# Kernel optimization log

Measured on AMD Instinct MI355X. Metric: run time of the kernel, lower is better.

Reference implementation:

```python
import jax, jax.numpy as jnp
import numpy as np
import math

# Static config derived from init_kwargs
B, L, D, H, NL = 256, 256, 128, 2, 2
E = D // H                       # 64
F = L // 2 + 1                   # 129 rfft bins
SR = 0.6                         # sample_ratio (> 1/n_layers)
STEP = (F * (1.0 - SR)) // (NL - 1)          # 51.0, python float floor-div as in torch code
LEFTS = [int(F * (1.0 - SR) - k * STEP) for k in range(NL)]   # [51, 0]
RIGHTS = [int(F - k * STEP) for k in range(NL)]               # [129, 78]
TOPK = max(int(1 * math.log(L)), 1)          # factor=1 -> 5
NUM_TOTAL = 100000                           # user_num + item_num
SPATIAL_RATIO = 0.1
INV_SQRT_E = 1.0 / math.sqrt(E)
INV_SQRT_2 = 1.0 / math.sqrt(2.0)


def setup_inputs() -> dict:
    key = jax.random.key(0)
    ks = jax.random.split(key, 12)
    s = 0.05
    return {
        "paths": jax.random.randint(ks[0], (B, L), 0, NUM_TOTAL),
        "lengths": jax.random.randint(ks[1], (B,), 1, L + 1),
        "degrees": jax.random.randint(ks[2], (B,), 0, 64),
        "training": 1,
        "ego_emb": jax.random.normal(ks[3], (NUM_TOTAL + 1, D), jnp.float32) * s,
        "pos_emb": jax.random.normal(ks[4], (L, D), jnp.float32) * s,
        "Wq": jax.random.normal(ks[5], (NL, D, D), jnp.float32) * s,
        "Wk": jax.random.normal(ks[6], (NL, D, D), jnp.float32) * s,
        "Wv": jax.random.normal(ks[7], (NL, D, D), jnp.float32) * s,
        "Wp": jax.random.normal(ks[8], (NL, D, D), jnp.float32) * s,
        "F1": jax.random.normal(ks[9], (NL, D, 2 * D), jnp.float32) * s,
        "F2": jax.random.normal(ks[10], (NL, 2 * D, D), jnp.float32) * s,
    }


def _hybrid_attention(k, x, mask, Wq, Wk, Wv, Wp):
    # project and split heads: [B,H,E,L]
    def proj(W):
        return (x @ W).reshape(B, L, H, E).transpose(0, 2, 3, 1)
    q, kk, v = proj(Wq), proj(Wk), proj(Wv)
    qf = jnp.fft.rfft(q, axis=-1)   # [B,H,E,F] complex
    kf = jnp.fft.rfft(kk, axis=-1)
    vf = jnp.fft.rfft(v, axis=-1)
    l, r = LEFTS[k], RIGHTS[k]
    # frequency-band attention: band-limited cross-correlation (scatter back == zero-pad)
    res = qf[..., l:r] * jnp.conj(kf[..., l:r])
    box = jnp.zeros(qf.shape, dtype=res.dtype).at[..., l:r].set(res)
    corr = jnp.fft.irfft(box, n=L, axis=-1)          # [B,H,E,L]
    mean_value = jnp.mean(corr, axis=(1, 2))         # [B,L]
    # training branch: global topk delays (shared across batch), roll-based aggregation
    _, delays = jax.lax.top_k(jnp.mean(mean_value, axis=0), TOPK)   # [TOPK]
    weights = mean_value[:, delays]                  # [B,TOPK]
    tmp_corr = jax.nn.softmax(weights, axis=-1)      # [B,TOPK]
    # roll(v, -d) along time == gather at (t + d) % L
    idx = (jnp.arange(L)[None, :] + delays[:, None]) % L            # [TOPK,L]
    gathered = v[:, :, :, idx]                       # [B,H,E,TOPK,L]
    freq = jnp.einsum('bhetl,bt->bhel', gathered, tmp_corr)
    freq = freq.transpose(0, 3, 1, 2).reshape(B, L, D)
    # dual-domain: time attention on band-limited signals (std=True -> same band)
    def band_ifft(f):
        padded = jnp.zeros(f.shape, dtype=f.dtype).at[..., l:r].set(f[..., l:r])
        return jnp.fft.irfft(padded, n=L, axis=-1).transpose(0, 1, 3, 2)   # [B,H,L,E]
    qt, kt, vt = band_ifft(qf), band_ifft(kf), band_ifft(vf)
    scores = jnp.einsum('bhqe,bhke->bhqk', qt, kt) * INV_SQRT_E + mask
    att = jax.nn.softmax(scores, axis=-1)
    spatial = jnp.einsum('bhqk,bhke->bhqe', att, vt).transpose(0, 2, 1, 3).reshape(B, L, D)
    out = (1.0 - SPATIAL_RATIO) * freq + SPATIAL_RATIO * spatial
    return out @ Wp + x


def reference(paths, lengths, degrees, training, ego_emb, pos_emb, Wq, Wk, Wv, Wp, F1, F2):
    del degrees, training  # degrees unused; training branch baked in (training=True)
    x = ego_emb[paths] + pos_emb[None, :, :]         # [B,L,D]
    m = (paths < NUM_TOTAL).astype(jnp.float32)
    mask = ((1.0 - m) * -10000.0)[:, None, None, :]  # [B,1,1,L]
    for k in range(NL):
        a = _hybrid_attention(k, x, mask, Wq[k], Wk[k], Wv[k], Wp[k])
        h = a @ F1[k]
        h = h * 0.5 * (1.0 + jax.lax.erf(h * INV_SQRT_2))   # exact GELU
        x = h @ F2[k]
    # gather last valid position per sequence
    return x[jnp.arange(B), lengths - 1]             # [B,D]
```

## Files before the change

### kernel.cpp

```cpp
#include <hip/hip_runtime.h>
#include <math.h>

#define Bn 256
#define Ln 256
#define Dn 128
#define Hn 2
#define En 64
#define NLn 2
#define TOPKn 5
#define NUM_TOTALn 100000
#define BLD (Bn*Ln*Dn)
#define WT_LAYER 147456

using frag_ab = __attribute__((ext_vector_type(8))) short;
using frag_cd = __attribute__((ext_vector_type(4))) float;

__device__ inline short f2bf(float f) {
    union { float f; unsigned u; } c; c.f = f;
    unsigned r = (c.u + 0x7FFFu + ((c.u >> 16) & 1u)) >> 16;
    return (short)r;
}
__device__ inline float bf2f(short s) {
    union { unsigned u; float f; } c; c.u = ((unsigned)(unsigned short)s) << 16;
    return c.f;
}

__global__ void beacon_kernel(float* out, float v) { out[0] = v; }

__global__ __launch_bounds__(256) void build_G_kernel(short* __restrict__ G) {
    int k = blockIdx.x, t = blockIdx.y, s = threadIdx.x;
    int d = (t - s) & 255;
    int f1 = (k == 0) ? 51 : 1;
    int f2 = (k == 0) ? 127 : 77;
    float acc;
    if (d == 0) {
        acc = 2.0f * (float)(f2 - f1 + 1);
    } else {
        const float c = 3.14159265358979323846f / 256.0f;
        int ahi = (d * (2 * f2 + 1)) & 511;
        int alo = (d * (2 * f1 - 1)) & 511;
        acc = (sinf(c * (float)ahi) - sinf(c * (float)alo)) / sinf(c * (float)d);
    }
    acc += (k == 0) ? ((d & 1) ? -1.0f : 1.0f)
                    : 1.0f;
    G[((size_t)k * 256 + t) * 256 + s] = f2bf(acc * (1.0f / 256.0f));
}

__global__ __launch_bounds__(256) void build_x_kernel(const int* __restrict__ paths,
                                                      const float* __restrict__ ego,
                                                      const float* __restrict__ pos,
                                                      short* __restrict__ x) {
    int base = (blockIdx.x * 256 + threadIdx.x) * 4;
    int d = base & 127;
    int bl = base >> 7;
    int t = bl & 255;
    float4 e = *(const float4*)(ego + (size_t)paths[bl] * Dn + d);
    float4 p = *(const float4*)(pos + t * Dn + d);
    short4 s;
    s.x = f2bf(e.x + p.x); s.y = f2bf(e.y + p.y);
    s.z = f2bf(e.z + p.z); s.w = f2bf(e.w + p.w);
    *(short4*)&x[base] = s;
}

__global__ __launch_bounds__(256) void wtrans_all_kernel(
        const float* __restrict__ Wq, const float* __restrict__ Wk,
        const float* __restrict__ Wv, const float* __restrict__ Wp,
        const float* __restrict__ F1, const float* __restrict__ F2,
        short* __restrict__ Wt) {
    int z = blockIdx.y;
    int idx = blockIdx.x * 256 + threadIdx.x;
    short* WtL = Wt + (size_t)z * WT_LAYER;
    if (idx < 65536) {
        int which = idx >> 14, local = idx & 16383;
        const float* src = (which == 0) ? Wq : (which == 1) ? Wk
                         : (which == 2) ? Wv : Wp;
        float scale = (which == 3) ? 0.1f : 1.0f;
        int n = local & 127, k = local >> 7;
        WtL[(which << 14) + n * 128 + k] = f2bf(scale * src[(size_t)z * 16384 + local]);
    } else if (idx < 98304) {
        int local = idx - 65536;
        int n = local & 255, k = local >> 8;
        WtL[65536 + n * 128 + k] = f2bf(F1[(size_t)z * 32768 + local]);
    } else {
        int local = idx - 98304;
        int n = local & 127, k = local >> 7;
        WtL[98304 + n * 256 + k] = f2bf(F2[(size_t)z * 32768 + local]);
    }
}

template<bool BT_FAST, bool GELU_EPI>
__global__ __launch_bounds__(256)
void mfma_gemm_kernel(const short* A, const short* Bp, short* C, const short* R,
                      int K, int lda, int ldb, int ldc, int ldr,
                      long long sA, long long sB, long long sC, long long sR,
                      long long sCsplit, float alpha, float beta) {
    int bz = blockIdx.z;
    A += (size_t)bz * sA; C += (size_t)bz * sC;
    if (R) R += (size_t)bz * sR;
    const short* Bt = Bp + (size_t)bz * sB;
    const int m0 = blockIdx.x * 128, n0 = blockIdx.y * 128;
    int n0c = n0;
    if (sCsplit) { C += (size_t)blockIdx.y * sCsplit; n0c = 0; }
    __shared__ short As[128 * 40];
    __shared__ short Bs[128 * 40];
    int tid = threadIdx.x;
    int lane = tid & 63, wave = tid >> 6;
    int wr = (wave >> 1) * 64, wc = (wave & 1) * 64;
    int l15 = lane & 15, qd = lane >> 4;

    frag_cd zero4 = {0.f, 0.f, 0.f, 0.f};
    frag_cd acc[4][4];
    #pragma unroll
    for (int i = 0; i < 4; i++)
        #pragma unroll
        for (int j = 0; j < 4; j++) acc[i][j] = zero4;

    int arow = tid >> 1, acg = (tid & 1) * 16;
    int bnrow = tid >> 1, bcg = (tid & 1) * 16;
    int bkk = tid & 31, bnb = (tid >> 5) * 16;

    int4 pa0, pa1, pb0, pb1;
    {
        const short* ap = A + (size_t)(m0 + arow) * lda + acg;
        pa0 = *(const int4*)ap; pa1 = *(const int4*)(ap + 8);
        if (BT_FAST) {
            const short* bp = Bt + (size_t)(n0 + bnrow) * ldb + bcg;
            pb0 = *(const int4*)bp; pb1 = *(const int4*)(bp + 8);
        } else {
            const short* bp = Bt + (size_t)bkk * ldb + n0 + bnb;
            pb0 = *(const int4*)bp; pb1 = *(const int4*)(bp + 8);
        }
    }

    for (int k0 = 0; k0 < K; k0 += 32) {
        __syncthreads();
        *(int4*)&As[arow * 40 + acg] = pa0;
        *(int4*)&As[arow * 40 + acg + 8] = pa1;
        if (BT_FAST) {
            *(int4*)&Bs[bnrow * 40 + bcg] = pb0;
            *(int4*)&Bs[bnrow * 40 + bcg + 8] = pb1;
        } else {
            short tmp[16];
            *(int4*)&tmp[0] = pb0; *(int4*)&tmp[8] = pb1;
            #pragma unroll
            for (int i = 0; i < 16; i++) Bs[(bnb + i) * 40 + bkk] = tmp[i];
        }
        __syncthreads();
        if (k0 + 32 < K) {
            const short* ap = A + (size_t)(m0 + arow) * lda + k0 + 32 + acg;
            pa0 = *(const int4*)ap; pa1 = *(const int4*)(ap + 8);
            if (BT_FAST) {
                const short* bp = Bt + (size_t)(n0 + bnrow) * ldb + k0 + 32 + bcg;
                pb0 = *(const int4*)bp; pb1 = *(const int4*)(bp + 8);
            } else {
                const short* bp = Bt + (size_t)(k0 + 32 + bkk) * ldb + n0 + bnb;
                pb0 = *(const int4*)bp; pb1 = *(const int4*)(bp + 8);
            }
        }
        frag_ab af[4], bf[4];
        #pragma unroll
        for (int ms = 0; ms < 4; ms++)
            af[ms] = *(frag_ab*)&As[(wr + ms * 16 + l15) * 40 + qd * 8];
        #pragma unroll
        for (int ns = 0; ns < 4; ns++)
            bf[ns] = *(frag_ab*)&Bs[(wc + ns * 16 + l15) * 40 + qd * 8];
        #pragma unroll
        for (int ms = 0; ms < 4; ms++)
            #pragma unroll
            for (int ns = 0; ns < 4; ns++)
                acc[ms][ns] = __builtin_amdgcn_mfma_f32_16x16x32_bf16(
                    bf[ns], af[ms], acc[ms][ns], 0, 0, 0);
    }
    #pragma unroll
    for (int ms = 0; ms < 4; ms++) {
        int m = m0 + wr + ms * 16 + l15;
        #pragma unroll
        for (int ns = 0; ns < 4; ns++) {
            int nb = wc + ns * 16 + qd * 4;
            float v[4];
            #pragma unroll
            for (int r = 0; r < 4; r++) v[r] = alpha * acc[ms][ns][r];
            if (R) {
                short4 r4 = *(const short4*)&R[(size_t)m * ldr + n0 + nb];
                v[0] += beta * bf2f(r4.x); v[1] += beta * bf2f(r4.y);
                v[2] += beta * bf2f(r4.z); v[3] += beta * bf2f(r4.w);
            }
            if (GELU_EPI) {
                #pragma unroll
                for (int r = 0; r < 4; r++)
                    v[r] = v[r] * 0.5f * (1.0f + erff(v[r] * 0.70710678118654752f));
            }
            short4 o;
            o.x = f2bf(v[0]); o.y = f2bf(v[1]); o.z = f2bf(v[2]); o.w = f2bf(v[3]);
            *(short4*)&C[(size_t)m * ldc + n0c + nb] = o;
        }
    }
}

static inline void mgemm(hipStream_t s, const short* A, const short* B, short* C,
                         const short* R, int M, int N, int K,
                         int lda, int ldb, int ldc, int ldr,
                         long long sA, long long sB, long long sC, long long sR,
                         int batch, float alpha, float beta, bool btFast, bool gelu,
                         long long sCsplit = 0) {
    dim3 grid(M / 128, N / 128, batch), block(256);
    if (btFast) {
        if (gelu) mfma_gemm_kernel<true, true ><<<grid, block, 0, s>>>(A, B, C, R, K, lda, ldb, ldc, ldr, sA, sB, sC, sR, sCsplit, alpha, beta);
        else      mfma_gemm_kernel<true, false><<<grid, block, 0, s>>>(A, B, C, R, K, lda, ldb, ldc, ldr, sA, sB, sC, sR, sCsplit, alpha, beta);
    } else {
        if (gelu) mfma_gemm_kernel<false, true ><<<grid, block, 0, s>>>(A, B, C, R, K, lda, ldb, ldc, ldr, sA, sB, sC, sR, sCsplit, alpha, beta);
        else      mfma_gemm_kernel<false, false><<<grid, block, 0, s>>>(A, B, C, R, K, lda, ldb, ldc, ldr, sA, sB, sC, sR, sCsplit, alpha, beta);
    }
}

template<bool DUAL, bool GELU_EPI, bool MIXA>
__global__ __launch_bounds__(512)
void bgemm_kernel(const short* __restrict__ A1, const short* __restrict__ B1, int K1,
                  const short* __restrict__ A2, const short* __restrict__ B2, int K2,
                  short* C, const short* __restrict__ R, int ldc, int ldr,
                  long long sCsplit,
                  const float* __restrict__ tc, const int* __restrict__ delays) {
    const int m0 = blockIdx.x * 256;
    int n0c;
    if (sCsplit) { C += (size_t)blockIdx.y * sCsplit; n0c = 0; }
    else         { n0c = blockIdx.y * 128; }
    __shared__ short As[256 * 40];
    __shared__ short Bs[128 * 40];
    int tid = threadIdx.x;
    int lane = tid & 63, wave = tid >> 6;
    int wr = (wave & 3) * 64, wc = (wave >> 2) * 64;
    int l15 = lane & 15, qd = lane >> 4;

    float wj[TOPKn]; int dj[TOPKn];
    if (MIXA) {
        #pragma unroll
        for (int j = 0; j < TOPKn; j++) {
            wj[j] = tc[blockIdx.x * TOPKn + j];
            dj[j] = delays[j];
        }
    }

    frag_cd zero4 = {0.f, 0.f, 0.f, 0.f};
    frag_cd acc[4][4];
    #pragma unroll
    for (int i = 0; i < 4; i++)
        #pragma unroll
        for (int j = 0; j < 4; j++) acc[i][j] = zero4;

    int arow = tid >> 1, acg = (tid & 1) * 16;
    int brow = tid >> 2, bcg = (tid & 3) * 8;

    #pragma unroll
    for (int pass = 0; pass < (DUAL ? 2 : 1); pass++) {
        const short* A = pass ? A2 : A1;
        const short* Bb = (pass ? B2 : B1);
        int K = pass ? K2 : K1;
        const bool domix = MIXA && (pass == 0);
        const short* Bt = Bb + (size_t)blockIdx.y * 128 * K;
        const short* xb = A + ((size_t)m0 << 7);
        int4 pa0, pa1, pb0;
        {
            if (!domix) {
                const short* ap = A + (size_t)(m0 + arow) * K + acg;
                pa0 = *(const int4*)ap; pa1 = *(const int4*)(ap + 8);
            }
            pb0 = *(const int4*)(Bt + (size_t)brow * K + bcg);
        }
        for (int k0 = 0; k0 < K; k0 += 32) {
            __syncthreads();
            if (domix) {
                #pragma unroll
                for (int c = 0; c < 2; c++) {
                    int col = k0 + acg + c * 8;
                    float m8[8] = {0.f, 0.f, 0.f, 0.f, 0.f, 0.f, 0.f, 0.f};
                    #pragma unroll
                    for (int j = 0; j < TOPKn; j++) {
                        frag_ab v = *(const frag_ab*)(xb + (((arow + dj[j]) & 255) << 7) + col);
                        #pragma unroll
                        for (int i = 0; i < 8; i++) m8[i] += wj[j] * bf2f(v[i]);
                    }
                    frag_ab o;
                    #pragma unroll
                    for (int i = 0; i < 8; i++) o[i] = f2bf(m8[i]);
                    *(frag_ab*)&As[arow * 40 + acg + c * 8] = o;
                }
            } else {
                *(int4*)&As[arow * 40 + acg] = pa0;
                *(int4*)&As[arow * 40 + acg + 8] = pa1;
            }
            *(int4*)&Bs[brow * 40 + bcg] = pb0;
            __syncthreads();
            if (k0 + 32 < K) {
                if (!domix) {
                    const short* ap = A + (size_t)(m0 + arow) * K + k0 + 32 + acg;
                    pa0 = *(const int4*)ap; pa1 = *(const int4*)(ap + 8);
                }
                pb0 = *(const int4*)(Bt + (size_t)brow * K + k0 + 32 + bcg);
            }
            frag_ab af[4], bf[4];
            #pragma unroll
            for (int ms = 0; ms < 4; ms++)
                af[ms] = *(frag_ab*)&As[(wr + ms * 16 + l15) * 40 + qd * 8];
            #pragma unroll
            for (int ns = 0; ns < 4; ns++)
                bf[ns] = *(frag_ab*)&Bs[(wc + ns * 16 + l15) * 40 + qd * 8];
            #pragma unroll
            for (int ms = 0; ms < 4; ms++)
                #pragma unroll
                for (int ns = 0; ns < 4; ns++)
                    acc[ms][ns] = __builtin_amdgcn_mfma_f32_16x16x32_bf16(
                        bf[ns], af[ms], acc[ms][ns], 0, 0, 0);
        }
    }
    #pragma unroll
    for (int ms = 0; ms < 4; ms++) {
        int m = m0 + wr + ms * 16 + l15;
        #pragma unroll
        for (int ns = 0; ns < 4; ns++) {
            int nb = wc + ns * 16 + qd * 4;
            float v[4];
            #pragma unroll
            for (int r = 0; r < 4; r++) v[r] = acc[ms][ns][r];
            if (R) {
                short4 r4 = *(const short4*)&R[(size_t)m * ldr + n0c + nb];
                v[0] += bf2f(r4.x); v[1] += bf2f(r4.y);
                v[2] += bf2f(r4.z); v[3] += bf2f(r4.w);
            }
            if (GELU_EPI) {
                #pragma unroll
                for (int r = 0; r < 4; r++)
                    v[r] = v[r] * 0.5f * (1.0f + erff(v[r] * 0.70710678118654752f));
            }
            short4 o;
            o.x = f2bf(v[0]); o.y = f2bf(v[1]); o.z = f2bf(v[2]); o.w = f2bf(v[3]);
            *(short4*)&C[(size_t)m * ldc + n0c + nb] = o;
        }
    }
}

__global__ __launch_bounds__(512, 4) void attn_kernel(short* q,
        const short* __restrict__ kb, const short* __restrict__ vf,
        const int* __restrict__ paths, float* __restrict__ mv2) {
    int h = blockIdx.x, b = blockIdx.y;
    __shared__ short SB[256 * 72];
    __shared__ short ks[64 * 72];
    __shared__ short vT[80 * 72];
    __shared__ float masks[256];
    __shared__ float mvpart[512];
    int tid = threadIdx.x;
    int lane = tid & 63, wave = tid >> 6;
    int l15 = lane & 15, qd = lane >> 4;
    if (tid < 256) masks[tid] = (paths[b * 256 + tid] < NUM_TOTALn) ? 0.0f : -10000.0f;
    {
        int e0 = tid * 2;
        #pragma unroll
        for (int i = 0; i < 2; i++) {
            int e = e0 + i;
            int row = 64 + (e >> 6), col = e & 63;
            vT[row * 72 + col] = (row == 64) ? (short)0x3F80 : (short)0;
        }
    }
    short* qg = q + ((size_t)b << 15) + (size_t)h * 64;
    const short* kg = kb + ((size_t)b << 15) + (size_t)h * 64;
    const short* vg = vf + ((size_t)b << 15) + (size_t)h * 64;

    #pragma unroll
    for (int p = 0; p < 4; p++) {
        int chunk = p * 512 + tid;
        int r = chunk >> 3, cb = (chunk & 7) * 8;
        *(frag_ab*)&SB[r * 72 + cb] = *(const frag_ab*)(qg + (size_t)r * 128 + cb);
    }
    __syncthreads();
    int myrow = wave * 32;
    frag_ab aq[2][2];
    #pragma unroll
    for (int mt = 0; mt < 2; mt++)
        #pragma unroll
        for (int hf = 0; hf < 2; hf++)
            aq[mt][hf] = *(frag_ab*)&SB[(myrow + mt * 16 + l15) * 72 + hf * 32 + qd * 8];

    frag_cd zero4 = {0.f, 0.f, 0.f, 0.f};
    frag_cd oacc[2][5];
    #pragma unroll
    for (int mt = 0; mt < 2; mt++)
        #pragma unroll
        for (int et = 0; et < 5; et++) oacc[mt][et] = zero4;
    float macc = 0.0f;
    int tau = tid & 255, half = tid >> 8;

    for (int jt = 0; jt < 4; jt++) {
        __syncthreads();
        {
            int r = tid >> 3, cb = (tid & 7) * 8;
            *(frag_ab*)&ks[r * 72 + cb] =
                *(const frag_ab*)(kg + (size_t)(jt * 64 + r) * 128 + cb);
            frag_ab v8 = *(const frag_ab*)(vg + (size_t)(jt * 64 + r) * 128 + cb);
            #pragma unroll
            for (int i = 0; i < 8; i++) vT[(cb + i) * 72 + r] = v8[i];
        }
        __syncthreads();
        #pragma unroll
        for (int mt = 0; mt < 2; mt++) {
            #pragma unroll
            for (int nt = 0; nt < 4; nt++) {
                frag_ab b0 = *(frag_ab*)&ks[(nt * 16 + l15) * 72 + qd * 8];
                frag_ab b1 = *(frag_ab*)&ks[(nt * 16 + l15) * 72 + 32 + qd * 8];
                frag_cd c = zero4;
                c = __builtin_amdgcn_mfma_f32_16x16x32_bf16(aq[mt][0], b0, c, 0, 0, 0);
                c = __builtin_amdgcn_mfma_f32_16x16x32_bf16(aq[mt][1], b1, c, 0, 0, 0);
                int keyLocal = nt * 16 + l15;
                #pragma unroll
                for (int r = 0; r < 4; r++) {
                    int row = myrow + mt * 16 + qd * 4 + r;
                    int tt = (row - jt * 64 - keyLocal) & 255;
                    SB[tt * 66 + keyLocal] = f2bf(c[r] * 0.125f);
                }
            }
        }
        __syncthreads();
        {
            const int* SD32 = (const int*)&SB[tau * 66 + half * 32];
            #pragma unroll
            for (int i = 0; i < 16; i++) {
                int pk = SD32[i];
                macc += bf2f((short)(pk & 0xFFFF)) + bf2f((short)(pk >> 16));
            }
        }
        #pragma unroll
        for (int mt = 0; mt < 2; mt++) {
            int row = myrow + mt * 16 + l15;
            #pragma unroll
            for (int hf = 0; hf < 2; hf++) {
                int kl0 = hf * 32 + qd * 8;
                frag_ab pfrag;
                #pragma unroll
                for (int j = 0; j < 8; j++) {
                    int kl = kl0 + j;
                    int tt = (row - jt * 64 - kl) & 255;
                    float s = bf2f(SB[tt * 66 + kl]);
                    pfrag[j] = f2bf(__expf(s + masks[jt * 64 + kl]));
                }
                #pragma unroll
                for (int et = 0; et < 5; et++) {
                    frag_ab bv = *(frag_ab*)&vT[(et * 16 + l15) * 72 + hf * 32 + qd * 8];
                    oacc[mt][et] = __builtin_amdgcn_mfma_f32_16x16x32_bf16(pfrag, bv, oacc[mt][et], 0, 0, 0);
                }
            }
        }
    }
    __syncthreads();
    mvpart[tid] = macc;
    __syncthreads();
    if (tid < 256)
        mv2[(size_t)h * 65536 + b * 256 + tid] =
            (mvpart[tid] + mvpart[tid + 256]) * 0.0625f;
    #pragma unroll
    for (int mt = 0; mt < 2; mt++) {
        #pragma unroll
        for (int r = 0; r < 4; r++) {
            float l = oacc[mt][4][r];
            l = __shfl(l, (lane & 48));
            float inv = 1.0f / l;
            int row = myrow + mt * 16 + qd * 4 + r;
            #pragma unroll
            for (int et = 0; et < 4; et++)
                qg[(size_t)row * 128 + et * 16 + l15] = f2bf(oacc[mt][et][r] * inv);
        }
    }
}

__global__ __launch_bounds__(256) void gm_reduce_kernel(const float* __restrict__ mv2,
                                                        float* __restrict__ gm) {
    int tau = blockIdx.x;
    int b = threadIdx.x;
    __shared__ float red[256];
    red[b] = mv2[b * 256 + tau] + mv2[65536 + b * 256 + tau];
    __syncthreads();
    for (int s = 128; s > 0; s >>= 1) { if (b < s) red[b] += red[b + s]; __syncthreads(); }
    if (b == 0) gm[tau] = red[0] * (1.0f / 256.0f);
}

__global__ __launch_bounds__(256) void topk_softmax_kernel(const float* __restrict__ gm,
                                                           const float* __restrict__ mv2,
                                                           int* __restrict__ delays,
                                                           float* __restrict__ tc) {
    __shared__ float vsh[4];
    __shared__ int ish[4];
    __shared__ int dsh[TOPKn];
    int tid = threadIdx.x;
    int lane = tid & 63, wave = tid >> 6;
    float v = gm[tid];
    for (int t = 0; t < TOPKn; t++) {
        float mv_ = v; int mi = tid;
        #pragma unroll
        for (int s = 32; s > 0; s >>= 1) {
            float v2 = __shfl_xor(mv_, s); int i2 = __shfl_xor(mi, s);
            if (v2 > mv_ || (v2 == mv_ && i2 < mi)) { mv_ = v2; mi = i2; }
        }
        if (lane == 0) { vsh[wave] = mv_; ish[wave] = mi; }
        __syncthreads();
        if (tid == 0) {
            float bv = vsh[0]; int bi = ish[0];
            #pragma unroll
            for (int w = 1; w < 4; w++)
                if (vsh[w] > bv || (vsh[w] == bv && ish[w] < bi)) { bv = vsh[w]; bi = ish[w]; }
            dsh[t] = bi; delays[t] = bi;
        }
        __syncthreads();
        if (tid == dsh[t]) v = -1e30f;
    }
    __syncthreads();
    int b = tid;
    float w[TOPKn];
    float m = -1e30f;
    #pragma unroll
    for (int j = 0; j < TOPKn; j++) {
        w[j] = mv2[b * 256 + dsh[j]] + mv2[65536 + b * 256 + dsh[j]];
        m = fmaxf(m, w[j]);
    }
    float ssum = 0.0f;
    #pragma unroll
    for (int j = 0; j < TOPKn; j++) { w[j] = expf(w[j] - m); ssum += w[j]; }
    #pragma unroll
    for (int j = 0; j < TOPKn; j++) tc[b * TOPKn + j] = w[j] / ssum;
}

__global__ __launch_bounds__(256) void gather_out_kernel(const short* __restrict__ x,
                                                         const int* __restrict__ lengths,
                                                         float* __restrict__ out) {
    int idx = blockIdx.x * 256 + threadIdx.x;
    int d = idx & 127;
    int b = idx >> 7;
    out[idx] = bf2f(x[((size_t)b << 15) + (size_t)(lengths[b] - 1) * Dn + d]);
}

extern "C" void kernel_launch(void* const* d_in, const int* in_sizes, int n_in,
                              void* d_out, int out_size, void* d_ws, size_t ws_size,
                              hipStream_t stream) {
    const int* paths    = (const int*)d_in[0];
    const int* lengths  = (const int*)d_in[1];
    const float* ego    = (const float*)d_in[4];
    const float* pos    = (const float*)d_in[5];
    const float* Wq     = (const float*)d_in[6];
    const float* Wk     = (const float*)d_in[7];
    const float* Wv     = (const float*)d_in[8];
    const float* Wp     = (const float*)d_in[9];
    const float* F1     = (const float*)d_in[10];
    const float* F2     = (const float*)d_in[11];
    float* out = (float*)d_out;

    const size_t need = (size_t)5 * BLD * 2 + 131072 * 2 + 131072 * 4
                        + 256 * 4 + 1280 * 4 + 16 * 4 + (size_t)NLn * WT_LAYER * 2;
    if (ws_size < need) {
        beacon_kernel<<<dim3(1), dim3(1), 0, stream>>>(out, (float)(ws_size >> 20));
        return;
    }

    short* x    = (short*)d_ws;
    short* q    = x + (size_t)1 * BLD;
    short* kb   = x + (size_t)2 * BLD;
    short* vf   = x + (size_t)3 * BLD;
    short* x5   = x + (size_t)4 * BLD;
    short* Gb   = x + (size_t)5 * BLD;
    float* mv   = (float*)(Gb + 131072);
    float* gm   = mv + 131072;
    float* tc   = gm + 256;
    int* delays = (int*)(tc + 1280);
    short* Wt   = (short*)(delays + 16);

    build_G_kernel<<<dim3(2, 256), dim3(256), 0, stream>>>(Gb);
    build_x_kernel<<<dim3(BLD / 1024), dim3(256), 0, stream>>>(paths, ego, pos, x);

    wtrans_all_kernel<<<dim3(512, NLn), dim3(256), 0, stream>>>(Wq, Wk, Wv, Wp, F1, F2, Wt);
    mgemm(stream, Wt + 49152, Wt + 32768, Wt + 131072, nullptr,
          128, 128, 128, 128, 128, 128, 0,
          WT_LAYER, WT_LAYER, WT_LAYER, 0, NLn,
          9.0f, 0.0f, false, false);

    for (int k = 0; k < NLn; k++) {
        const short* WtL = Wt + (size_t)k * WT_LAYER;
        mgemm(stream, Gb + (size_t)k * 65536, x, x5, nullptr,
              256, 128, 256, 256, 128, 128, 0,
              0, 32768, 32768, 0, 256, 1.0f, 0.0f, false, false);
        bgemm_kernel<false, false, false><<<dim3(256, 3), dim3(512), 0, stream>>>(
            x5, WtL + 0, 128, nullptr, nullptr, 0, q, nullptr, 128, 0,
            (long long)BLD, nullptr, nullptr);

        attn_kernel<<<dim3(2, 256), dim3(512), 0, stream>>>(q, kb, vf, paths, mv);

        gm_reduce_kernel<<<dim3(256), dim3(256), 0, stream>>>(mv, gm);
        topk_softmax_kernel<<<dim3(1), dim3(256), 0, stream>>>(gm, mv, delays, tc);

        bgemm_kernel<true, false, true><<<dim3(256, 1), dim3(512), 0, stream>>>(
            x, WtL + 131072, 128, q, WtL + 49152, 128, kb, x, 128, 128, 0,
            tc, delays);
        bgemm_kernel<false, true, false><<<dim3(256, 2), dim3(512), 0, stream>>>(
            kb, WtL + 65536, 128, nullptr, nullptr, 0, vf, nullptr, 256, 0, 0,
            nullptr, nullptr);
        bgemm_kernel<false, false, false><<<dim3(256, 1), dim3(512), 0, stream>>>(
            vf, WtL + 98304, 256, nullptr, nullptr, 0, x, nullptr, 128, 0, 0,
            nullptr, nullptr);
    }

    gather_out_kernel<<<dim3((Bn * Dn) / 256), dim3(256), 0, stream>>>(x, lengths, out);
}
```

Before: 398.4 us.

## Compute softmax denominator in registers and use ballot mask bits in attention

Drops the extra ones-column MFMA tile that produced the softmax row sum. The row sum is now accumulated in registers from the bf16 probabilities and reduced with lane shuffles. The float mask array becomes 64-bit ballot bitmasks, so masked keys are zeroed directly and their exp is skipped. Q fragments are loaded straight from global memory instead of being staged through shared memory, and the loops are reordered so each K fragment and V fragment feeds two MFMAs; together these cut shared memory use and MFMA count, at the cost of more VALU work for the row sums.

```diff
diff --git a/kernel.cpp b/kernel.cpp
--- a/kernel.cpp
+++ b/kernel.cpp
@@ -342,49 +342,40 @@
         const short* __restrict__ kb, const short* __restrict__ vf,
         const int* __restrict__ paths, float* __restrict__ mv2) {
     int h = blockIdx.x, b = blockIdx.y;
-    __shared__ short SB[256 * 72];
+    __shared__ short SD[256 * 66];
     __shared__ short ks[64 * 72];
-    __shared__ short vT[80 * 72];
-    __shared__ float masks[256];
+    __shared__ short vT[64 * 72];
     __shared__ float mvpart[512];
+    __shared__ unsigned long long mbits[4];
     int tid = threadIdx.x;
     int lane = tid & 63, wave = tid >> 6;
     int l15 = lane & 15, qd = lane >> 4;
-    if (tid < 256) masks[tid] = (paths[b * 256 + tid] < NUM_TOTALn) ? 0.0f : -10000.0f;
-    {
-        int e0 = tid * 2;
-        #pragma unroll
-        for (int i = 0; i < 2; i++) {
-            int e = e0 + i;
-            int row = 64 + (e >> 6), col = e & 63;
-            vT[row * 72 + col] = (row == 64) ? (short)0x3F80 : (short)0;
-        }
-    }
+
+    if (wave < 4) {
+        unsigned long long mb = __ballot(paths[b * 256 + tid] < NUM_TOTALn);
+        if (lane == 0) mbits[wave] = mb;
+    }
+
     short* qg = q + ((size_t)b << 15) + (size_t)h * 64;
     const short* kg = kb + ((size_t)b << 15) + (size_t)h * 64;
     const short* vg = vf + ((size_t)b << 15) + (size_t)h * 64;
 
-    #pragma unroll
-    for (int p = 0; p < 4; p++) {
-        int chunk = p * 512 + tid;
-        int r = chunk >> 3, cb = (chunk & 7) * 8;
-        *(frag_ab*)&SB[r * 72 + cb] = *(const frag_ab*)(qg + (size_t)r * 128 + cb);
-    }
-    __syncthreads();
     int myrow = wave * 32;
     frag_ab aq[2][2];
     #pragma unroll
     for (int mt = 0; mt < 2; mt++)
         #pragma unroll
         for (int hf = 0; hf < 2; hf++)
-            aq[mt][hf] = *(frag_ab*)&SB[(myrow + mt * 16 + l15) * 72 + hf * 32 + qd * 8];
+            aq[mt][hf] = *(const frag_ab*)(qg
+                + (size_t)(myrow + mt * 16 + l15) * 128 + hf * 32 + qd * 8);
 
     frag_cd zero4 = {0.f, 0.f, 0.f, 0.f};
-    frag_cd oacc[2][5];
+    frag_cd oacc[2][4];
     #pragma unroll
     for (int mt = 0; mt < 2; mt++)
         #pragma unroll
-        for (int et = 0; et < 5; et++) oacc[mt][et] = zero4;
+        for (int et = 0; et < 4; et++) oacc[mt][et] = zero4;
+    float dsum[2] = {0.f, 0.f};
     float macc = 0.0f;
     int tau = tid & 255, half = tid >> 8;
 
@@ -400,51 +391,59 @@
         }
         __syncthreads();
         #pragma unroll
-        for (int mt = 0; mt < 2; mt++) {
-            #pragma unroll
-            for (int nt = 0; nt < 4; nt++) {
-                frag_ab b0 = *(frag_ab*)&ks[(nt * 16 + l15) * 72 + qd * 8];
-                frag_ab b1 = *(frag_ab*)&ks[(nt * 16 + l15) * 72 + 32 + qd * 8];
+        for (int nt = 0; nt < 4; nt++) {
+            frag_ab b0 = *(frag_ab*)&ks[(nt * 16 + l15) * 72 + qd * 8];
+            frag_ab b1 = *(frag_ab*)&ks[(nt * 16 + l15) * 72 + 32 + qd * 8];
+            int keyLocal = nt * 16 + l15;
+            #pragma unroll
+            for (int mt = 0; mt < 2; mt++) {
                 frag_cd c = zero4;
                 c = __builtin_amdgcn_mfma_f32_16x16x32_bf16(aq[mt][0], b0, c, 0, 0, 0);
                 c = __builtin_amdgcn_mfma_f32_16x16x32_bf16(aq[mt][1], b1, c, 0, 0, 0);
-                int keyLocal = nt * 16 + l15;
                 #pragma unroll
                 for (int r = 0; r < 4; r++) {
                     int row = myrow + mt * 16 + qd * 4 + r;
                     int tt = (row - jt * 64 - keyLocal) & 255;
-                    SB[tt * 66 + keyLocal] = f2bf(c[r] * 0.125f);
+                    SD[tt * 66 + keyLocal] = f2bf(c[r] * 0.125f);
                 }
             }
         }
         __syncthreads();
         {
-            const int* SD32 = (const int*)&SB[tau * 66 + half * 32];
+            const int* SD32 = (const int*)&SD[tau * 66 + half * 32];
             #pragma unroll
             for (int i = 0; i < 16; i++) {
                 int pk = SD32[i];
                 macc += bf2f((short)(pk & 0xFFFF)) + bf2f((short)(pk >> 16));
             }
         }
-        #pragma unroll
-        for (int mt = 0; mt < 2; mt++) {
-            int row = myrow + mt * 16 + l15;
-            #pragma unroll
-            for (int hf = 0; hf < 2; hf++) {
+        unsigned long long mk = mbits[jt];
+        #pragma unroll
+        for (int hf = 0; hf < 2; hf++) {
+            frag_ab pf[2];
+            #pragma unroll
+            for (int mt = 0; mt < 2; mt++) {
+                int row = myrow + mt * 16 + l15;
                 int kl0 = hf * 32 + qd * 8;
                 frag_ab pfrag;
+                float ds = 0.f;
                 #pragma unroll
                 for (int j = 0; j < 8; j++) {
                     int kl = kl0 + j;
                     int tt = (row - jt * 64 - kl) & 255;
-                    float s = bf2f(SB[tt * 66 + kl]);
-                    pfrag[j] = f2bf(__expf(s + masks[jt * 64 + kl]));
+                    float s = bf2f(SD[tt * 66 + kl]);
+                    short pb = ((mk >> kl) & 1ull) ? f2bf(__expf(s)) : (short)0;
+                    pfrag[j] = pb;
+                    ds += bf2f(pb);
                 }
-                #pragma unroll
-                for (int et = 0; et < 5; et++) {
-                    frag_ab bv = *(frag_ab*)&vT[(et * 16 + l15) * 72 + hf * 32 + qd * 8];
-                    oacc[mt][et] = __builtin_amdgcn_mfma_f32_16x16x32_bf16(pfrag, bv, oacc[mt][et], 0, 0, 0);
-                }
+                dsum[mt] += ds;
+                pf[mt] = pfrag;
+            }
+            #pragma unroll
+            for (int et = 0; et < 4; et++) {
+                frag_ab bv = *(frag_ab*)&vT[(et * 16 + l15) * 72 + hf * 32 + qd * 8];
+                oacc[0][et] = __builtin_amdgcn_mfma_f32_16x16x32_bf16(pf[0], bv, oacc[0][et], 0, 0, 0);
+                oacc[1][et] = __builtin_amdgcn_mfma_f32_16x16x32_bf16(pf[1], bv, oacc[1][et], 0, 0, 0);
             }
         }
     }
@@ -456,10 +455,17 @@
             (mvpart[tid] + mvpart[tid + 256]) * 0.0625f;
     #pragma unroll
     for (int mt = 0; mt < 2; mt++) {
+        float d = dsum[mt];
+        d += __shfl_xor(d, 16);
+        d += __shfl_xor(d, 32);
+        dsum[mt] = d;
+    }
+    #pragma unroll
+    for (int mt = 0; mt < 2; mt++) {
         #pragma unroll
         for (int r = 0; r < 4; r++) {
-            float l = oacc[mt][4][r];
-            l = __shfl(l, (lane & 48));
+            int srcl = (lane & 48) | (qd * 4 + r);
+            float l = __shfl(dsum[mt], srcl);
             float inv = 1.0f / l;
             int row = myrow + mt * 16 + qd * 4 + r;
             #pragma unroll
```

After: 446.5 us. 1.12x slower.
